# Optimization experiments

Measured on AMD Instinct MI355X. Metric: run time of the kernel, lower is better.

## Reference

```python
import jax, jax.numpy as jnp
import numpy as np

NUM_HEADS = 8
HEAD_DIM = 128
NUM_HIDDEN = 2048  # memory slots per head
D_MODEL = 1024
B, S = 1, 4096
EPS = 1e-6


def _normalize(kq):
    ss = jnp.sum(jnp.square(kq), axis=-1, keepdims=True)
    return kq * jax.lax.rsqrt(ss + EPS)


def setup_inputs() -> dict:
    key = jax.random.key(0)
    ks = jax.random.split(key, 5)
    x = jax.random.normal(ks[0], (B, S, D_MODEL), dtype=jnp.float32)
    # variance_scaling fan_in ~ stddev 1/sqrt(fan_in); plain normal is fine for a baseline
    Wq = jax.random.normal(ks[1], (D_MODEL, NUM_HEADS * HEAD_DIM), dtype=jnp.float32) / np.sqrt(D_MODEL)
    keys = jax.random.normal(ks[2], (NUM_HIDDEN * NUM_HEADS, HEAD_DIM), dtype=jnp.float32)
    values = jax.random.normal(ks[3], (NUM_HIDDEN * NUM_HEADS, HEAD_DIM), dtype=jnp.float32)
    attn_scale = jnp.ones((NUM_HEADS,), dtype=jnp.float32)
    Wo = jax.random.normal(ks[4], (NUM_HEADS * HEAD_DIM, D_MODEL), dtype=jnp.float32) / np.sqrt(NUM_HEADS * HEAD_DIM)
    return {"x": x, "Wq": Wq, "keys": keys, "values": values, "attn_scale": attn_scale, "Wo": Wo}


def reference(x, Wq, keys, values, attn_scale, Wo):
    # reshape memory bank: (k*h, d) -> (k, h, d)
    k = keys.reshape(NUM_HIDDEN, NUM_HEADS, HEAD_DIM)
    v = values.reshape(NUM_HIDDEN, NUM_HEADS, HEAD_DIM)
    # query projection, split heads: [B,S,h*d] -> [B,S,h,d]
    q = jnp.einsum('bsm,mn->bsn', x, Wq).reshape(B, S, NUM_HEADS, HEAD_DIM)
    # L2-normalize keys and queries; fold learned per-head scale into keys
    k = _normalize(k) * attn_scale.reshape(1, NUM_HEADS, 1)
    q = _normalize(q)
    # attention against fixed memory bank: [B,S,h,k]
    attn = jnp.einsum('bshd,khd->bshk', q, k)
    attn = jax.nn.softmax(attn, axis=-1)
    # read values: [B,S,h,d] -> merge heads -> output projection
    y = jnp.einsum('bshk,khd->bshd', attn, v).reshape(B, S, NUM_HEADS * HEAD_DIM)
    return jnp.einsum('bsn,no->bso', y, Wo)
```

## Files before the change

### kernel.cpp

```cpp
#include <hip/hip_runtime.h>
#include <math.h>

#define S_LEN 4096
#define DM 1024
#define NHEADS 8
#define HDIM 128
#define NSLOTS 2048

typedef __attribute__((ext_vector_type(8))) short bf16x8;
typedef __attribute__((ext_vector_type(4))) float f32x4;
typedef __attribute__((ext_vector_type(16))) float f32x16;
typedef __attribute__((ext_vector_type(4))) unsigned u32x4;

static __device__ __forceinline__ unsigned short f2bf(float f) {
  union { float f; unsigned u; } v; v.f = f;
  unsigned u = v.u;
  return (unsigned short)((u + 0x7fffu + ((u >> 16) & 1u)) >> 16);
}
static __device__ __forceinline__ unsigned pack2(float a, float b) {
  return (unsigned)f2bf(a) | ((unsigned)f2bf(b) << 16);
}
static __device__ __forceinline__ f32x4 mfma16(bf16x8 a, bf16x8 b, f32x4 c) {
  return __builtin_amdgcn_mfma_f32_16x16x32_bf16(a, b, c, 0, 0, 0);
}
static __device__ __forceinline__ f32x16 mfma32(bf16x8 a, bf16x8 b, f32x16 c) {
  return __builtin_amdgcn_mfma_f32_32x32x16_bf16(a, b, c, 0, 0, 0);
}
static __device__ __forceinline__ void gll16(const void* g, void* l) {
  __builtin_amdgcn_global_load_lds(
      (__attribute__((address_space(1))) void*)(void*)(unsigned long long)(const char*)g,
      (__attribute__((address_space(3))) void*)l, 16, 0, 0);
}
static __device__ __forceinline__ float fexp2(float x) {
  float r;
  asm("v_exp_f32 %0, %1" : "=v"(r) : "v"(x));
  return r;
}


__global__ __launch_bounds__(256) void prep_kernel(
    const float* __restrict__ x, const float* __restrict__ Wq,
    const float* __restrict__ Wo, const float* __restrict__ keys,
    const float* __restrict__ values, const float* __restrict__ scale,
    unsigned short* __restrict__ xb, unsigned short* __restrict__ wqt,
    unsigned short* __restrict__ wot, unsigned* __restrict__ kbf_w,
    unsigned short* __restrict__ vt) {
  __shared__ float tileU[64 * 129];
  int b = blockIdx.x, t = threadIdx.x;

  if (b < 1024) {
    int mb = b >> 4, kb64 = b & 15;
#pragma unroll
    for (int p = 0; p < 4; p++) {
      int fi = t + 256 * p;
      int row = fi >> 4, kq = fi & 15;
      float4 v = *(const float4*)(x + ((size_t)(mb * 64 + row) * DM + kb64 * 64 + kq * 4));
      float* d = &tileU[row * 65 + kq * 4];
      d[0] = v.x; d[1] = v.y; d[2] = v.z; d[3] = v.w;
    }
    __syncthreads();
#pragma unroll
    for (int p2 = 0; p2 < 2; p2++) {
      int g = t + 256 * p2;
      int kb = g >> 6, row = g & 63;
      const float* src = &tileU[row * 65 + kb * 8];
      u32x4 w;
#pragma unroll
      for (int q = 0; q < 4; q++) w[q] = pack2(src[2 * q], src[2 * q + 1]);
      *(u32x4*)(xb + ((size_t)(mb * 16 + kb64) * 8 + kb) * 512 + row * 8) = w;
    }
  } else if (b < 1280) {
    int b2 = b - 1024;
    const float* W = (b2 < 128) ? Wq : Wo;
    unsigned short* WT = (b2 < 128) ? wqt : wot;
    int r = b2 & 127;
    int nb = r >> 4, kb64 = r & 15;
#pragma unroll
    for (int p = 0; p < 8; p++) {
      int fi = t + 256 * p;
      int krow = fi >> 5, nq = fi & 31;
      float4 v = *(const float4*)(W + ((size_t)(kb64 * 64 + krow) * DM + nb * 128 + nq * 4));
      float* d = &tileU[krow * 129 + nq * 4];
      d[0] = v.x; d[1] = v.y; d[2] = v.z; d[3] = v.w;
    }
    __syncthreads();
#pragma unroll
    for (int p2 = 0; p2 < 4; p2++) {
      int g = t + 256 * p2;
      int pp = g >> 6, r6 = g & 63;
      int kb = pp >> 1, rh = pp & 1;
      u32x4 w;
#pragma unroll
      for (int q = 0; q < 4; q++)
        w[q] = pack2(tileU[(kb * 8 + 2 * q) * 129 + rh * 64 + r6],
                     tileU[(kb * 8 + 2 * q + 1) * 129 + rh * 64 + r6]);
      *(u32x4*)(WT + ((size_t)(nb * 16 + kb64) * 16 + pp) * 512 + r6 * 8) = w;
    }
  } else if (b < 5376) {
    int b3 = b - 1280;
    int w = b3 * 4 + (t >> 6);
    int lane = t & 63;
    int slot = w >> 3, h = w & 7;
    float2 v = ((const float2*)(keys + (size_t)w * HDIM))[lane];
    float ss = v.x * v.x + v.y * v.y;
#pragma unroll
    for (int m = 1; m < 64; m <<= 1) ss += __shfl_xor(ss, m);
    float sc = scale[h] * rsqrtf(ss + 1e-6f);
    size_t off = (size_t)h * 131072 + (slot >> 6) * 4096 +
                 (((slot >> 5) & 1) * 8 + (lane >> 3)) * 256 + ((lane >> 2) & 1) * 128 +
                 (slot & 31) * 4 + (lane & 3);
    kbf_w[off] = pack2(v.x * sc, v.y * sc);
  } else {
    int b4 = b - 5376;
    int h = b4 >> 5, c = b4 & 31;
#pragma unroll
    for (int p = 0; p < 8; p++) {
      int fi = t + 256 * p;
      int srow = fi >> 5, dq = fi & 31;
      float4 v = *(const float4*)(values +
                                  ((size_t)((c * 64 + srow) * NHEADS + h) * HDIM + dq * 4));
      float* d = &tileU[srow * 129 + dq * 4];
      d[0] = v.x; d[1] = v.y; d[2] = v.z; d[3] = v.w;
    }
    __syncthreads();
#pragma unroll
    for (int p2 = 0; p2 < 4; p2++) {
      int g = t + 256 * p2;
      int sb = g >> 7, d = g & 127;
      u32x4 w;
#pragma unroll
      for (int q = 0; q < 4; q++)
        w[q] = pack2(tileU[(sb * 8 + 2 * q) * 129 + d], tileU[(sb * 8 + 2 * q + 1) * 129 + d]);
      *(u32x4*)(vt + (size_t)h * 262144 + c * 8192 + (sb * 128 + d) * 8) = w;
    }
  }
}

template <bool FUSE_QNORM>
__global__ __launch_bounds__(256) void gemm_nt_kernel(const unsigned short* __restrict__ A,
                                                      const unsigned short* __restrict__ Bt,
                                                      float* __restrict__ Cf,
                                                      unsigned short* __restrict__ Cq,
                                                      int M, int N, int K) {
  __shared__ __align__(16) unsigned short As2[2][4096];
  __shared__ __align__(16) unsigned short Bs2[2][8192];
  __shared__ float ssq[64][2];
  int t = threadIdx.x;
  int wave = t >> 6, lane = t & 63;
  int l16 = lane & 15, quad = lane >> 4;
  int m_blk = blockIdx.y * 64, n_blk = blockIdx.x * 128;
  int wm = (wave & 1) * 32, wn = (wave >> 1) * 64;
  int nk64 = K >> 6;
  f32x4 zero = {0.f, 0.f, 0.f, 0.f};
  f32x4 acc[2][4];
#pragma unroll
  for (int i = 0; i < 2; i++)
#pragma unroll
    for (int j = 0; j < 4; j++) acc[i][j] = zero;

  auto stage = [&](int k0, int b) {
    int kb64 = k0 >> 6;
    const unsigned short* Abase = A + ((size_t)(blockIdx.y * nk64 + kb64)) * 4096;
    const unsigned short* Bbase = Bt + ((size_t)(blockIdx.x * nk64 + kb64)) * 8192;
#pragma unroll
    for (int i = 0; i < 2; i++) {
      int kb = wave * 2 + i;
      gll16(Abase + kb * 512 + lane * 8, &As2[b][kb * 512]);
    }
#pragma unroll
    for (int i = 0; i < 4; i++) {
      int j = wave * 4 + i;
      gll16(Bbase + j * 512 + lane * 8, &Bs2[b][j * 512]);
    }
  };

  stage(0, 0);
  for (int k0 = 0; k0 < K; k0 += 64) {
    int b = (k0 >> 6) & 1;
    __syncthreads();
    if (k0 + 64 < K) stage(k0 + 64, b ^ 1);
#pragma unroll
    for (int kk = 0; kk < 2; kk++) {
      bf16x8 af[2], bfr[4];
#pragma unroll
      for (int mt = 0; mt < 2; mt++)
        af[mt] = *(const bf16x8*)&As2[b][((kk * 4 + quad) * 64 + wm + mt * 16 + l16) * 8];
#pragma unroll
      for (int nt = 0; nt < 4; nt++)
        bfr[nt] = *(const bf16x8*)&Bs2[b][((kk * 4 + quad) * 128 + wn + nt * 16 + l16) * 8];
#pragma unroll
      for (int mt = 0; mt < 2; mt++)
#pragma unroll
        for (int nt = 0; nt < 4; nt++) acc[mt][nt] = mfma16(af[mt], bfr[nt], acc[mt][nt]);
    }
  }

  if (FUSE_QNORM) {
#pragma unroll
    for (int mt = 0; mt < 2; mt++)
#pragma unroll
      for (int r = 0; r < 4; r++) {
        float s = 0.f;
#pragma unroll
        for (int nt = 0; nt < 4; nt++) s += acc[mt][nt][r] * acc[mt][nt][r];
#pragma unroll
        for (int d = 1; d < 16; d <<= 1) s += __shfl_xor(s, d);
        if (l16 == 0) ssq[wm + mt * 16 + quad * 4 + r][wave >> 1] = s;
      }
    __syncthreads();
#pragma unroll
    for (int mt = 0; mt < 2; mt++)
#pragma unroll
      for (int r = 0; r < 4; r++) {
        int row = wm + mt * 16 + quad * 4 + r;
        float rs = rsqrtf(ssq[row][0] + ssq[row][1] + 1e-6f) * 1.44269504f;
#pragma unroll
        for (int nt = 0; nt < 4; nt++)
          Cq[(size_t)(m_blk + row) * N + n_blk + wn + nt * 16 + l16] =
              f2bf(acc[mt][nt][r] * rs);
      }
  } else {
#pragma unroll
    for (int mt = 0; mt < 2; mt++)
#pragma unroll
      for (int nt = 0; nt < 4; nt++)
#pragma unroll
        for (int r = 0; r < 4; r++)
          Cf[(size_t)(m_blk + wm + mt * 16 + quad * 4 + r) * N + n_blk + wn + nt * 16 +
             l16] = acc[mt][nt][r];
  }
}

__global__ __launch_bounds__(256, 2) void attn_kernel(const unsigned short* __restrict__ qbf,
                                                      const unsigned short* __restrict__ kbf,
                                                      const unsigned short* __restrict__ vt,
                                                      const float* __restrict__ scale,
                                                      unsigned short* __restrict__ yb) {
  __shared__ __align__(16) char smem[59392];
  unsigned short(*Ks)[8192] = (unsigned short(*)[8192])smem;
  unsigned short* Vs = (unsigned short*)(smem + 32768);
  unsigned short(*pbuf)[32][40] = (unsigned short(*)[32][40])(smem + 49152);
  int h = blockIdx.x, t = threadIdx.x;
  int wave = t >> 6, lane = t & 63;
  int l32 = lane & 31, h8 = lane >> 5;
  int g = wave >> 1, s = wave & 1;
  int q0 = blockIdx.y * 64 + g * 32;
  const unsigned short* Kh = kbf + (size_t)h * 262144;
  const unsigned short* Vh = vt + (size_t)h * 262144;
  float M2 = fabsf(scale[h]) * 1.44269504f;

  bf16x8 aq[8];
  const unsigned short* qrow = qbf + (size_t)(q0 + l32) * DM + h * HDIM + h8 * 8;
#pragma unroll
  for (int dt = 0; dt < 8; dt++) aq[dt] = *(const bf16x8*)(qrow + dt * 16);

  f32x16 zero16 = {};
  f32x16 O[4];
#pragma unroll
  for (int i = 0; i < 4; i++) O[i] = zero16;
  float lsum[16];
#pragma unroll
  for (int r = 0; r < 16; r++) lsum[r] = 0.f;

  auto stageK = [&](int c, int b) {
#pragma unroll
    for (int ii = 0; ii < 4; ii++) {
      int j = wave * 4 + ii;
      gll16(Kh + (size_t)c * 8192 + j * 512 + lane * 8, &Ks[b][j * 512]);
    }
  };
  auto stageV = [&](int c) {
#pragma unroll
    for (int ii = 0; ii < 4; ii++) {
      int j = wave * 4 + ii;
      gll16(Vh + (size_t)c * 8192 + j * 512 + lane * 8, &Vs[j * 512]);
    }
  };

  constexpr int NC = NSLOTS / 64;
  stageK(0, 0);
  for (int c = 0; c < NC; c++) {
    int b = c & 1;
    __syncthreads();
    if (c + 1 < NC) stageK(c + 1, b ^ 1);
    stageV(c);

    f32x16 acc0 = zero16, acc1 = zero16;
#pragma unroll
    for (int dt = 0; dt < 4; dt++) {
      bf16x8 k0 = *(const bf16x8*)&Ks[b][s * 4096 + ((4 * dt + h8) * 32 + l32) * 8];
      bf16x8 k1 = *(const bf16x8*)&Ks[b][s * 4096 + ((4 * dt + 2 + h8) * 32 + l32) * 8];
      acc0 = mfma32(aq[2 * dt], k0, acc0);
      acc1 = mfma32(aq[2 * dt + 1], k1, acc1);
    }
    f32x16 acc = acc0 + acc1;
#pragma unroll
    for (int r = 0; r < 16; r++) {
      float p = fexp2(acc[r] - M2);
      lsum[r] += p;
      pbuf[wave][(r & 3) + 8 * (r >> 2) + 4 * h8][l32] = f2bf(p);
    }
    bf16x8 pa[2];
#pragma unroll
    for (int ks = 0; ks < 2; ks++)
      pa[ks] = *(const bf16x8*)&pbuf[wave][l32][ks * 16 + h8 * 8];

    __syncthreads();
#pragma unroll
    for (int nt = 0; nt < 4; nt++) {
      f32x16 o = O[nt];
      o = mfma32(pa[0], *(const bf16x8*)&Vs[((s * 4 + 0 + h8) * 128 + nt * 32 + l32) * 8], o);
      o = mfma32(pa[1], *(const bf16x8*)&Vs[((s * 4 + 2 + h8) * 128 + nt * 32 + l32) * 8], o);
      O[nt] = o;
    }
  }

  __syncthreads();
  float(*Oc)[32][128] = (float(*)[32][128])smem;
  float(*Lc)[32][32] = (float(*)[32][32])(smem + 32768);
  if (s == 1) {
#pragma unroll
    for (int nt = 0; nt < 4; nt++)
#pragma unroll
      for (int r = 0; r < 16; r++)
        Oc[g][(r & 3) + 8 * (r >> 2) + 4 * h8][nt * 32 + l32] = O[nt][r];
#pragma unroll
    for (int r = 0; r < 16; r++) Lc[g][(r & 3) + 8 * (r >> 2) + 4 * h8][l32] = lsum[r];
  }
  __syncthreads();
  if (s == 0) {
#pragma unroll
    for (int r = 0; r < 16; r++) {
      int row = (r & 3) + 8 * (r >> 2) + 4 * h8;
      float sum = lsum[r] + Lc[g][row][l32];
#pragma unroll
      for (int d = 1; d < 32; d <<= 1) sum += __shfl_xor(sum, d);
      float inv = 1.0f / sum;
#pragma unroll
      for (int nt = 0; nt < 4; nt++) {
        float v = O[nt][r] + Oc[g][row][nt * 32 + l32];
        size_t off = ((size_t)blockIdx.y * 16 + h * 2 + (nt >> 1)) * 4096 +
                     ((nt & 1) * 4 + (l32 >> 3)) * 512 + (g * 32 + row) * 8 + (l32 & 7);
        yb[off] = f2bf(v * inv);
      }
    }
  }
}


extern "C" void kernel_launch(void* const* d_in, const int* in_sizes, int n_in,
                              void* d_out, int out_size, void* d_ws, size_t ws_size,
                              hipStream_t stream) {
  const float* x = (const float*)d_in[0];
  const float* Wq = (const float*)d_in[1];
  const float* keys = (const float*)d_in[2];
  const float* values = (const float*)d_in[3];
  const float* attn_scale = (const float*)d_in[4];
  const float* Wo = (const float*)d_in[5];
  float* out = (float*)d_out;

  char* ws = (char*)d_ws;
  unsigned short* xb = (unsigned short*)(ws);
  unsigned short* wqt = (unsigned short*)(ws + (8ull << 20));
  unsigned short* wot = (unsigned short*)(ws + (10ull << 20));
  unsigned short* kbf = (unsigned short*)(ws + (12ull << 20));
  unsigned short* vt = (unsigned short*)(ws + (16ull << 20));
  unsigned short* qbf = (unsigned short*)(ws + (20ull << 20));
  unsigned short* yb = (unsigned short*)(ws + (28ull << 20));

  prep_kernel<<<5632, 256, 0, stream>>>(x, Wq, Wo, keys, values, attn_scale, xb, wqt, wot,
                                        (unsigned*)kbf, vt);
  gemm_nt_kernel<true><<<dim3(8, 64), 256, 0, stream>>>(xb, wqt, nullptr, qbf,
                                                        S_LEN, DM, DM);
  attn_kernel<<<dim3(8, 64), 256, 0, stream>>>(qbf, kbf, vt, attn_scale, yb);
  gemm_nt_kernel<false><<<dim3(8, 64), 256, 0, stream>>>(yb, wot, out, nullptr,
                                                         S_LEN, DM, DM);
}
```

Before: 184.1 us.

## Double-buffer V, transpose QK MFMA, pass P via lane shuffles

Double-buffers the V tiles alongside K so that the loads for the next chunk overlap the current chunk's compute, which removes the mid-loop __syncthreads. The QK^T MFMA is transposed (K as the A operand) so each lane holds probabilities for one query row. The P operand is then built in registers with a cross-half shuffle instead of going through a shared-memory buffer, and the row sum shrinks to one scalar per lane. Shared memory grows to 64KB per block, which may limit occupancy at two blocks per CU.

```diff
diff --git a/kernel.cpp b/kernel.cpp
--- a/kernel.cpp
+++ b/kernel.cpp
@@ -236,10 +236,9 @@
                                                       const unsigned short* __restrict__ vt,
                                                       const float* __restrict__ scale,
                                                       unsigned short* __restrict__ yb) {
-  __shared__ __align__(16) char smem[59392];
+  __shared__ __align__(16) char smem[65536];
   unsigned short(*Ks)[8192] = (unsigned short(*)[8192])smem;
-  unsigned short* Vs = (unsigned short*)(smem + 32768);
-  unsigned short(*pbuf)[32][40] = (unsigned short(*)[32][40])(smem + 49152);
+  unsigned short(*Vs)[8192] = (unsigned short(*)[8192])(smem + 32768);
   int h = blockIdx.x, t = threadIdx.x;
   int wave = t >> 6, lane = t & 63;
   int l32 = lane & 31, h8 = lane >> 5;
@@ -258,9 +257,7 @@
   f32x16 O[4];
 #pragma unroll
   for (int i = 0; i < 4; i++) O[i] = zero16;
-  float lsum[16];
-#pragma unroll
-  for (int r = 0; r < 16; r++) lsum[r] = 0.f;
+  float lsum = 0.f;
 
   auto stageK = [&](int c, int b) {
 #pragma unroll
@@ -269,79 +266,96 @@
       gll16(Kh + (size_t)c * 8192 + j * 512 + lane * 8, &Ks[b][j * 512]);
     }
   };
-  auto stageV = [&](int c) {
+  auto stageV = [&](int c, int b) {
 #pragma unroll
     for (int ii = 0; ii < 4; ii++) {
       int j = wave * 4 + ii;
-      gll16(Vh + (size_t)c * 8192 + j * 512 + lane * 8, &Vs[j * 512]);
+      gll16(Vh + (size_t)c * 8192 + j * 512 + lane * 8, &Vs[b][j * 512]);
     }
   };
 
   constexpr int NC = NSLOTS / 64;
   stageK(0, 0);
+  stageV(0, 0);
   for (int c = 0; c < NC; c++) {
     int b = c & 1;
     __syncthreads();
-    if (c + 1 < NC) stageK(c + 1, b ^ 1);
-    stageV(c);
+    if (c + 1 < NC) {
+      stageK(c + 1, b ^ 1);
+      stageV(c + 1, b ^ 1);
+    }
 
     f32x16 acc0 = zero16, acc1 = zero16;
 #pragma unroll
     for (int dt = 0; dt < 4; dt++) {
-      bf16x8 k0 = *(const bf16x8*)&Ks[b][s * 4096 + ((4 * dt + h8) * 32 + l32) * 8];
-      bf16x8 k1 = *(const bf16x8*)&Ks[b][s * 4096 + ((4 * dt + 2 + h8) * 32 + l32) * 8];
-      acc0 = mfma32(aq[2 * dt], k0, acc0);
-      acc1 = mfma32(aq[2 * dt + 1], k1, acc1);
+      bf16x8 k0 = *(const bf16x8*)&Ks[b][s * 4096 + (2 * dt) * 512 + h8 * 256 + l32 * 8];
+      bf16x8 k1 = *(const bf16x8*)&Ks[b][s * 4096 + (2 * dt + 1) * 512 + h8 * 256 + l32 * 8];
+      acc0 = mfma32(k0, aq[2 * dt], acc0);
+      acc1 = mfma32(k1, aq[2 * dt + 1], acc1);
     }
     f32x16 acc = acc0 + acc1;
+
+    float p[16];
 #pragma unroll
     for (int r = 0; r < 16; r++) {
-      float p = fexp2(acc[r] - M2);
-      lsum[r] += p;
-      pbuf[wave][(r & 3) + 8 * (r >> 2) + 4 * h8][l32] = f2bf(p);
-    }
-    bf16x8 pa[2];
-#pragma unroll
-    for (int ks = 0; ks < 2; ks++)
-      pa[ks] = *(const bf16x8*)&pbuf[wave][l32][ks * 16 + h8 * 8];
-
-    __syncthreads();
-#pragma unroll
-    for (int nt = 0; nt < 4; nt++) {
-      f32x16 o = O[nt];
-      o = mfma32(pa[0], *(const bf16x8*)&Vs[((s * 4 + 0 + h8) * 128 + nt * 32 + l32) * 8], o);
-      o = mfma32(pa[1], *(const bf16x8*)&Vs[((s * 4 + 2 + h8) * 128 + nt * 32 + l32) * 8], o);
-      O[nt] = o;
-    }
-  }
+      p[r] = fexp2(acc[r] - M2);
+      lsum += p[r];
+    }
+    unsigned P2[8], U2[8];
+#pragma unroll
+    for (int i = 0; i < 8; i++) {
+      P2[i] = pack2(p[2 * i], p[2 * i + 1]);
+      U2[i] = (unsigned)__shfl_xor((int)P2[i], 32);
+    }
+    union PA { unsigned u[4]; bf16x8 v; };
+    PA pa[2];
+#pragma unroll
+    for (int kk = 0; kk < 2; kk++) {
+      int i0 = kk * 4 + h8 * 2;
+      pa[kk].u[0] = h8 ? U2[i0] : P2[i0];
+      pa[kk].u[1] = h8 ? U2[i0 + 1] : P2[i0 + 1];
+      pa[kk].u[2] = h8 ? P2[i0] : U2[i0];
+      pa[kk].u[3] = h8 ? P2[i0 + 1] : U2[i0 + 1];
+    }
+
+#pragma unroll
+    for (int dtile = 0; dtile < 4; dtile++) {
+      f32x16 o = O[dtile];
+#pragma unroll
+      for (int kk = 0; kk < 2; kk++) {
+        bf16x8 vf = *(const bf16x8*)&Vs[b][((s * 4 + kk * 2 + h8) * 128 + dtile * 32 + l32) * 8];
+        o = mfma32(pa[kk].v, vf, o);
+      }
+      O[dtile] = o;
+    }
+  }
+
+  float lsum_tot = lsum + __shfl_xor(lsum, 32);
 
   __syncthreads();
   float(*Oc)[32][128] = (float(*)[32][128])smem;
-  float(*Lc)[32][32] = (float(*)[32][32])(smem + 32768);
+  float(*Lc)[32] = (float(*)[32])(smem + 32768);
   if (s == 1) {
 #pragma unroll
-    for (int nt = 0; nt < 4; nt++)
+    for (int dtile = 0; dtile < 4; dtile++)
 #pragma unroll
       for (int r = 0; r < 16; r++)
-        Oc[g][(r & 3) + 8 * (r >> 2) + 4 * h8][nt * 32 + l32] = O[nt][r];
-#pragma unroll
-    for (int r = 0; r < 16; r++) Lc[g][(r & 3) + 8 * (r >> 2) + 4 * h8][l32] = lsum[r];
+        Oc[g][(r & 3) + 8 * (r >> 2) + 4 * h8][dtile * 32 + l32] = O[dtile][r];
+    if (h8 == 0) Lc[g][l32] = lsum_tot;
   }
   __syncthreads();
   if (s == 0) {
+    float inv = 1.0f / (lsum_tot + Lc[g][l32]);
 #pragma unroll
     for (int r = 0; r < 16; r++) {
       int row = (r & 3) + 8 * (r >> 2) + 4 * h8;
-      float sum = lsum[r] + Lc[g][row][l32];
-#pragma unroll
-      for (int d = 1; d < 32; d <<= 1) sum += __shfl_xor(sum, d);
-      float inv = 1.0f / sum;
-#pragma unroll
-      for (int nt = 0; nt < 4; nt++) {
-        float v = O[nt][r] + Oc[g][row][nt * 32 + l32];
-        size_t off = ((size_t)blockIdx.y * 16 + h * 2 + (nt >> 1)) * 4096 +
-                     ((nt & 1) * 4 + (l32 >> 3)) * 512 + (g * 32 + row) * 8 + (l32 & 7);
-        yb[off] = f2bf(v * inv);
+      float invr = __shfl(inv, row);
+#pragma unroll
+      for (int dtile = 0; dtile < 4; dtile++) {
+        float v = O[dtile][r] + Oc[g][row][dtile * 32 + l32];
+        size_t off = ((size_t)blockIdx.y * 16 + h * 2 + (dtile >> 1)) * 4096 +
+                     ((dtile & 1) * 4 + (l32 >> 3)) * 512 + (g * 32 + row) * 8 + (l32 & 7);
+        yb[off] = f2bf(v * invr);
       }
     }
   }
```

New measurement: 204.9 us. 11.3% more time.

## Split GEMM tile over 8 waves with 32-wide K steps

Applied to the files above, without the earlier changes.

The two projection GEMMs now run with 512 threads (8 waves) per 64x128 output tile instead of 4 waves, so each wave computes a 32x32 sub-tile. The K loop steps by 32 instead of 64, which halves the shared-memory staging buffers, and the q-norm partial sums are reduced across four column groups. The aim is more waves in flight and lower LDS and register use per block, to hide memory latency better. The cost is twice as many barriers per K and fewer MFMAs per fragment load.

```diff
diff --git a/kernel.cpp b/kernel.cpp
--- a/kernel.cpp
+++ b/kernel.cpp
@@ -137,75 +137,72 @@
 }
 
 template <bool FUSE_QNORM>
-__global__ __launch_bounds__(256) void gemm_nt_kernel(const unsigned short* __restrict__ A,
-                                                      const unsigned short* __restrict__ Bt,
-                                                      float* __restrict__ Cf,
-                                                      unsigned short* __restrict__ Cq,
-                                                      int M, int N, int K) {
-  __shared__ __align__(16) unsigned short As2[2][4096];
-  __shared__ __align__(16) unsigned short Bs2[2][8192];
-  __shared__ float ssq[64][2];
+__global__ __launch_bounds__(512, 4) void gemm_nt_kernel(const unsigned short* __restrict__ A,
+                                                         const unsigned short* __restrict__ Bt,
+                                                         float* __restrict__ Cf,
+                                                         unsigned short* __restrict__ Cq,
+                                                         int M, int N, int K) {
+  __shared__ __align__(16) unsigned short As2[2][2048];
+  __shared__ __align__(16) unsigned short Bs2[2][4096];
+  __shared__ float ssq[64][4];
   int t = threadIdx.x;
   int wave = t >> 6, lane = t & 63;
   int l16 = lane & 15, quad = lane >> 4;
   int m_blk = blockIdx.y * 64, n_blk = blockIdx.x * 128;
-  int wm = (wave & 1) * 32, wn = (wave >> 1) * 64;
+  int wm = (wave & 1) * 32, wn = (wave >> 1) * 32;
   int nk64 = K >> 6;
   f32x4 zero = {0.f, 0.f, 0.f, 0.f};
-  f32x4 acc[2][4];
+  f32x4 acc[2][2];
 #pragma unroll
   for (int i = 0; i < 2; i++)
 #pragma unroll
-    for (int j = 0; j < 4; j++) acc[i][j] = zero;
+    for (int j = 0; j < 2; j++) acc[i][j] = zero;
 
   auto stage = [&](int k0, int b) {
-    int kb64 = k0 >> 6;
+    int kb64 = k0 >> 6, half = (k0 >> 5) & 1;
     const unsigned short* Abase = A + ((size_t)(blockIdx.y * nk64 + kb64)) * 4096;
     const unsigned short* Bbase = Bt + ((size_t)(blockIdx.x * nk64 + kb64)) * 8192;
-#pragma unroll
-    for (int i = 0; i < 2; i++) {
-      int kb = wave * 2 + i;
-      gll16(Abase + kb * 512 + lane * 8, &As2[b][kb * 512]);
-    }
-#pragma unroll
-    for (int i = 0; i < 4; i++) {
-      int j = wave * 4 + i;
-      gll16(Bbase + j * 512 + lane * 8, &Bs2[b][j * 512]);
+    {
+      int i = wave >> 1, rh = wave & 1;
+      gll16(Bbase + (((half * 4 + i) * 2 + rh) * 512) + lane * 8, &Bs2[b][wave * 512]);
+    }
+    if (wave < 4) {
+      gll16(Abase + ((half * 4 + wave) * 512) + lane * 8, &As2[b][wave * 512]);
     }
   };
 
   stage(0, 0);
-  for (int k0 = 0; k0 < K; k0 += 64) {
-    int b = (k0 >> 6) & 1;
-    __syncthreads();
-    if (k0 + 64 < K) stage(k0 + 64, b ^ 1);
-#pragma unroll
-    for (int kk = 0; kk < 2; kk++) {
-      bf16x8 af[2], bfr[4];
-#pragma unroll
-      for (int mt = 0; mt < 2; mt++)
-        af[mt] = *(const bf16x8*)&As2[b][((kk * 4 + quad) * 64 + wm + mt * 16 + l16) * 8];
-#pragma unroll
-      for (int nt = 0; nt < 4; nt++)
-        bfr[nt] = *(const bf16x8*)&Bs2[b][((kk * 4 + quad) * 128 + wn + nt * 16 + l16) * 8];
-#pragma unroll
-      for (int mt = 0; mt < 2; mt++)
-#pragma unroll
-        for (int nt = 0; nt < 4; nt++) acc[mt][nt] = mfma16(af[mt], bfr[nt], acc[mt][nt]);
-    }
+  for (int k0 = 0; k0 < K; k0 += 32) {
+    int b = (k0 >> 5) & 1;
+    __syncthreads();
+    if (k0 + 32 < K) stage(k0 + 32, b ^ 1);
+    bf16x8 af[2], bfr[2];
+#pragma unroll
+    for (int mt = 0; mt < 2; mt++)
+      af[mt] = *(const bf16x8*)&As2[b][(quad * 64 + wm + mt * 16 + l16) * 8];
+#pragma unroll
+    for (int nt = 0; nt < 2; nt++) {
+      int n = wn + nt * 16 + l16;
+      bfr[nt] = *(const bf16x8*)&Bs2[b][((quad * 2 + (n >> 6)) * 64 + (n & 63)) * 8];
+    }
+#pragma unroll
+    for (int mt = 0; mt < 2; mt++)
+#pragma unroll
+      for (int nt = 0; nt < 2; nt++) acc[mt][nt] = mfma16(af[mt], bfr[nt], acc[mt][nt]);
   }
 
   if (FUSE_QNORM) {
+    int cg = wave >> 1;
 #pragma unroll
     for (int mt = 0; mt < 2; mt++)
 #pragma unroll
       for (int r = 0; r < 4; r++) {
         float s = 0.f;
 #pragma unroll
-        for (int nt = 0; nt < 4; nt++) s += acc[mt][nt][r] * acc[mt][nt][r];
+        for (int nt = 0; nt < 2; nt++) s += acc[mt][nt][r] * acc[mt][nt][r];
 #pragma unroll
         for (int d = 1; d < 16; d <<= 1) s += __shfl_xor(s, d);
-        if (l16 == 0) ssq[wm + mt * 16 + quad * 4 + r][wave >> 1] = s;
+        if (l16 == 0) ssq[wm + mt * 16 + quad * 4 + r][cg] = s;
       }
     __syncthreads();
 #pragma unroll
@@ -213,9 +210,10 @@
 #pragma unroll
       for (int r = 0; r < 4; r++) {
         int row = wm + mt * 16 + quad * 4 + r;
-        float rs = rsqrtf(ssq[row][0] + ssq[row][1] + 1e-6f) * 1.44269504f;
-#pragma unroll
-        for (int nt = 0; nt < 4; nt++)
+        float rs = rsqrtf(ssq[row][0] + ssq[row][1] + ssq[row][2] + ssq[row][3] + 1e-6f) *
+                   1.44269504f;
+#pragma unroll
+        for (int nt = 0; nt < 2; nt++)
           Cq[(size_t)(m_blk + row) * N + n_blk + wn + nt * 16 + l16] =
               f2bf(acc[mt][nt][r] * rs);
       }
@@ -223,7 +221,7 @@
 #pragma unroll
     for (int mt = 0; mt < 2; mt++)
 #pragma unroll
-      for (int nt = 0; nt < 4; nt++)
+      for (int nt = 0; nt < 2; nt++)
 #pragma unroll
         for (int r = 0; r < 4; r++)
           Cf[(size_t)(m_blk + wm + mt * 16 + quad * 4 + r) * N + n_blk + wn + nt * 16 +
@@ -370,9 +368,9 @@
 
   prep_kernel<<<5632, 256, 0, stream>>>(x, Wq, Wo, keys, values, attn_scale, xb, wqt, wot,
                                         (unsigned*)kbf, vt);
-  gemm_nt_kernel<true><<<dim3(8, 64), 256, 0, stream>>>(xb, wqt, nullptr, qbf,
+  gemm_nt_kernel<true><<<dim3(8, 64), 512, 0, stream>>>(xb, wqt, nullptr, qbf,
                                                         S_LEN, DM, DM);
   attn_kernel<<<dim3(8, 64), 256, 0, stream>>>(qbf, kbf, vt, attn_scale, yb);
-  gemm_nt_kernel<false><<<dim3(8, 64), 256, 0, stream>>>(yb, wot, out, nullptr,
+  gemm_nt_kernel<false><<<dim3(8, 64), 512, 0, stream>>>(yb, wot, out, nullptr,
                                                          S_LEN, DM, DM);
 }
```

After: 187.6 us. Within noise of the previous version (+1.9%).
